# Performance work log

Measured on AMD Instinct MI355X. Metric: run time of the kernel, lower is better.

## Reference

```python
import jax, jax.numpy as jnp
import numpy as np

D_K, D_V, H, N = 128, 256, 256, 50
B, L = 128, 1024

def setup_inputs() -> dict:
    key = jax.random.key(0)
    ks = jax.random.split(key, 10)
    s = lambda fan_in: 1.0 / np.sqrt(fan_in)
    return {
        'problems': jax.random.normal(ks[0], (B, L, D_K), dtype=jnp.float32),
        'interactions': jax.random.normal(ks[1], (B, L, D_V), dtype=jnp.float32),
        'w_key': jax.random.uniform(ks[2], (N, D_K), jnp.float32, -s(D_K), s(D_K)),
        'w_erase_w': jax.random.uniform(ks[3], (D_V, D_V), jnp.float32, -s(D_V), s(D_V)),
        'w_erase_b': jax.random.uniform(ks[4], (D_V,), jnp.float32, -s(D_V), s(D_V)),
        'w_add_w': jax.random.uniform(ks[5], (D_V, D_V), jnp.float32, -s(D_V), s(D_V)),
        'w_add_b': jax.random.uniform(ks[6], (D_V,), jnp.float32, -s(D_V), s(D_V)),
        'w_out_w': jax.random.uniform(ks[7], (H, D_V + D_K), jnp.float32, -s(D_V + D_K), s(D_V + D_K)),
        'w_out_b': jax.random.uniform(ks[8], (H,), jnp.float32, -s(D_V + D_K), s(D_V + D_K)),
        'init_memory': jax.random.normal(ks[9], (N, D_V), dtype=jnp.float32),
    }

def reference(problems, interactions, w_key, w_erase_w, w_erase_b, w_add_w, w_add_b, w_out_w, w_out_b, init_memory):
    # Precompute per-step gates outside the scan (they do not depend on memory)
    e = jax.nn.sigmoid(jnp.einsum('bld,ed->ble', interactions, w_erase_w) + w_erase_b)  # (B,L,d_v)
    a = jnp.tanh(jnp.einsum('bld,ed->ble', interactions, w_add_w) + w_add_b)            # (B,L,d_v)
    score = jax.nn.softmax(jnp.einsum('bld,nd->bln', problems, w_key), axis=-1)          # (B,L,n)

    mem0 = jnp.broadcast_to(init_memory, (problems.shape[0], N, D_V))

    def step(memory, xs):
        sc_t, e_t, a_t = xs  # (B,n), (B,d_v), (B,d_v)
        read = jnp.einsum('bn,bnd->bd', sc_t, memory)  # weighted read
        memory = memory * (1.0 - sc_t[:, :, None] * e_t[:, None, :])
        memory = memory + sc_t[:, :, None] * a_t[:, None, :]
        return memory, read

    xs = (score.transpose(1, 0, 2), e.transpose(1, 0, 2), a.transpose(1, 0, 2))  # time-major
    _, reads = jax.lax.scan(step, mem0, xs)  # reads: (L,B,d_v)

    x = jnp.concatenate([reads.transpose(1, 0, 2), problems], axis=-1)  # (B,L,d_v+d_k)
    # dropout in eval mode = identity
    return jnp.tanh(jnp.einsum('blc,hc->blh', x, w_out_w) + w_out_b)
```

## Files before the change

### kernel.cpp

```cpp
#include <hip/hip_runtime.h>

#define B_    128
#define L_    1024
#define DK_   128
#define DV_   256
#define NS_   50
#define H_    256
#define M_    (B_ * L_)

typedef __attribute__((ext_vector_type(8))) short   short8;
typedef __attribute__((ext_vector_type(4))) float   float4v;
typedef __attribute__((ext_vector_type(2))) float   float2v;
typedef __attribute__((ext_vector_type(4))) int     int4v;

__device__ __forceinline__ float b2f(unsigned short u) {
    unsigned int x = ((unsigned int)u) << 16;
    return __builtin_bit_cast(float, x);
}
__device__ __forceinline__ unsigned short f2b(float f) {
    unsigned int x = __builtin_bit_cast(unsigned int, f);
    x += 0x7fffu + ((x >> 16) & 1u);
    return (unsigned short)(x >> 16);
}
__device__ __forceinline__ int pack2(float lo, float hi) {
    return (int)f2b(lo) | ((int)f2b(hi) << 16);
}
__device__ __forceinline__ float sigmoid_f(float x) {
    return 1.f / (1.f + __expf(-x));
}
__device__ __forceinline__ float tanh_f(float x) {
    return 1.f - 2.f / (__expf(2.f * x) + 1.f);
}

__global__ __launch_bounds__(256) void gate_kernel(
    const float* __restrict__ X,
    const float* __restrict__ We, const float* __restrict__ be,
    const float* __restrict__ Wa, const float* __restrict__ ba,
    unsigned short* __restrict__ e_out, unsigned short* __restrict__ a_out)
{
    constexpr int K = DV_;
    const int mblk = blockIdx.x, nblk = blockIdx.y, gate = blockIdx.z;
    const float* W    = gate ? Wa : We;
    const float* bias = gate ? ba : be;
    unsigned short* out = gate ? a_out : e_out;

    __shared__ unsigned short As[128 * 40];
    __shared__ unsigned short Bs[128 * 40];

    const int tid  = threadIdx.x;
    const int lane = tid & 63, wid = tid >> 6;
    const int wm = wid >> 1, wn = wid & 1;
    const int l15 = lane & 15, quad = lane >> 4;

    float4v acc[4][4];
#pragma unroll
    for (int i = 0; i < 4; i++)
#pragma unroll
        for (int j = 0; j < 4; j++) {
            acc[i][j][0] = 0.f; acc[i][j][1] = 0.f;
            acc[i][j][2] = 0.f; acc[i][j][3] = 0.f;
        }

    const int srow = tid >> 1;
    const int scol = (tid & 1) * 16;
    const size_t Abase = ((size_t)mblk * 128 + srow) * K;
    const size_t Bbase = ((size_t)nblk * 128 + srow) * K;

    for (int k0 = 0; k0 < K; k0 += 32) {
        const float* xa = &X[Abase + k0 + scol];
        const float* xb = &W[Bbase + k0 + scol];
        float4v va0 = *(const float4v*)(xa);
        float4v va1 = *(const float4v*)(xa + 4);
        float4v va2 = *(const float4v*)(xa + 8);
        float4v va3 = *(const float4v*)(xa + 12);
        float4v vb0 = *(const float4v*)(xb);
        float4v vb1 = *(const float4v*)(xb + 4);
        float4v vb2 = *(const float4v*)(xb + 8);
        float4v vb3 = *(const float4v*)(xb + 12);
        int4v pa0, pa1, pb0, pb1;
        pa0[0] = pack2(va0[0], va0[1]); pa0[1] = pack2(va0[2], va0[3]);
        pa0[2] = pack2(va1[0], va1[1]); pa0[3] = pack2(va1[2], va1[3]);
        pa1[0] = pack2(va2[0], va2[1]); pa1[1] = pack2(va2[2], va2[3]);
        pa1[2] = pack2(va3[0], va3[1]); pa1[3] = pack2(va3[2], va3[3]);
        pb0[0] = pack2(vb0[0], vb0[1]); pb0[1] = pack2(vb0[2], vb0[3]);
        pb0[2] = pack2(vb1[0], vb1[1]); pb0[3] = pack2(vb1[2], vb1[3]);
        pb1[0] = pack2(vb2[0], vb2[1]); pb1[1] = pack2(vb2[2], vb2[3]);
        pb1[2] = pack2(vb3[0], vb3[1]); pb1[3] = pack2(vb3[2], vb3[3]);
        *(int4v*)&As[srow * 40 + scol]     = pa0;
        *(int4v*)&As[srow * 40 + scol + 8] = pa1;
        *(int4v*)&Bs[srow * 40 + scol]     = pb0;
        *(int4v*)&Bs[srow * 40 + scol + 8] = pb1;
        __syncthreads();
        short8 af[4], bf[4];
#pragma unroll
        for (int i = 0; i < 4; i++)
            af[i] = *(const short8*)&As[(64 * wm + 16 * i + l15) * 40 + quad * 8];
#pragma unroll
        for (int j = 0; j < 4; j++)
            bf[j] = *(const short8*)&Bs[(64 * wn + 16 * j + l15) * 40 + quad * 8];
#pragma unroll
        for (int i = 0; i < 4; i++)
#pragma unroll
            for (int j = 0; j < 4; j++)
                acc[i][j] = __builtin_amdgcn_mfma_f32_16x16x32_bf16(af[i], bf[j], acc[i][j], 0, 0, 0);
        __syncthreads();
    }

#pragma unroll
    for (int i = 0; i < 4; i++) {
        const int row = mblk * 128 + 64 * wm + 16 * i + quad * 4;
#pragma unroll
        for (int j = 0; j < 4; j++) {
            const int col = nblk * 128 + 64 * wn + 16 * j + l15;
            const float bv = bias[col];
#pragma unroll
            for (int r = 0; r < 4; r++) {
                float v = acc[i][j][r] + bv;
                v = gate ? tanh_f(v) : sigmoid_f(v);
                out[(size_t)(row + r) * DV_ + col] = f2b(v);
            }
        }
    }
}

__global__ __launch_bounds__(256) void score_kernel(
    const float* __restrict__ problems,
    const float* __restrict__ w_key,
    float* __restrict__ score_scan)
{
    const int rowi = blockIdx.x * 256 + threadIdx.x;
    const float* p = problems + (size_t)rowi * DK_;

    float logit[NS_];
#pragma unroll
    for (int n = 0; n < NS_; n++) logit[n] = 0.f;

    for (int k0 = 0; k0 < DK_; k0 += 4) {
        float pf0 = p[k0], pf1 = p[k0+1], pf2 = p[k0+2], pf3 = p[k0+3];
#pragma unroll
        for (int n = 0; n < NS_; n++) {
            const float* wk = &w_key[n * DK_ + k0];
            logit[n] += pf0 * wk[0] + pf1 * wk[1] + pf2 * wk[2] + pf3 * wk[3];
        }
    }

    float mx = logit[0];
#pragma unroll
    for (int n = 1; n < NS_; n++) mx = fmaxf(mx, logit[n]);
    float sum = 0.f;
#pragma unroll
    for (int n = 0; n < NS_; n++) { logit[n] = __expf(logit[n] - mx); sum += logit[n]; }
    const float inv = 1.f / sum;

    float* o = score_scan + (size_t)rowi * 64;
#pragma unroll
    for (int v = 0; v < 16; v++) {
        float4v st;
#pragma unroll
        for (int c = 0; c < 4; c++) {
            const int j = v * 4 + c;
            st[c] = (j < NS_) ? logit[j] * inv : 0.f;
        }
        *(float4v*)(o + v * 4) = st;
    }
}

#define RCH 16

__global__ __launch_bounds__(512, 4) void scan_kernel(
    const float* __restrict__ score_scan,
    const unsigned short* __restrict__ e_buf,
    const unsigned short* __restrict__ a_buf,
    const float* __restrict__ init_mem,
    unsigned short* __restrict__ reads)
{
    __shared__ float r_s[8][RCH][64];

    const int b    = blockIdx.y;
    const int dblk = blockIdx.x;
    const int tid  = threadIdx.x;
    const int w    = tid >> 6;
    const int lane = tid & 63;
    const int d    = dblk * 64 + lane;

    float M[8];
#pragma unroll
    for (int i = 0; i < 8; i++) {
        const int n = w * 8 + i;
        M[i] = (n < NS_) ? init_mem[n * DV_ + d] : 0.f;
    }

    const size_t rb = (size_t)b * L_;
    const float* sbase = score_scan + rb * 64 + w * 8;
    const unsigned short* ep = e_buf + rb * DV_ + d;
    const unsigned short* ap = a_buf + rb * DV_ + d;

    float s_p[4][8];
    unsigned short e_p[8], a_p[8];

#pragma unroll
    for (int k = 0; k < 4; k++) {
        const float* sp = sbase + (size_t)k * 64;
        float4v x0 = *(const float4v*)(sp);
        float4v x1 = *(const float4v*)(sp + 4);
        s_p[k][0] = x0[0]; s_p[k][1] = x0[1]; s_p[k][2] = x0[2]; s_p[k][3] = x0[3];
        s_p[k][4] = x1[0]; s_p[k][5] = x1[1]; s_p[k][6] = x1[2]; s_p[k][7] = x1[3];
    }
#pragma unroll
    for (int k = 0; k < 8; k++) {
        e_p[k] = ep[(size_t)k * DV_];
        a_p[k] = ap[(size_t)k * DV_];
    }

    for (int t0 = 0; t0 < L_; t0 += RCH) {
#pragma unroll
        for (int u = 0; u < RCH; u++) {
            const float e_cur = b2f(e_p[u & 7]);
            const float a_cur = b2f(a_p[u & 7]);
            float r = 0.f;
#pragma unroll
            for (int i = 0; i < 8; i++) {
                const float s = s_p[u & 3][i];
                r = fmaf(s, M[i], r);
                M[i] = fmaf(s, fmaf(-e_cur, M[i], a_cur), M[i]);
            }
            r_s[w][u][lane] = r;
            {
                const float* sp = sbase + (size_t)(t0 + u + 4) * 64;
                float4v x0 = *(const float4v*)(sp);
                float4v x1 = *(const float4v*)(sp + 4);
                s_p[u & 3][0] = x0[0]; s_p[u & 3][1] = x0[1];
                s_p[u & 3][2] = x0[2]; s_p[u & 3][3] = x0[3];
                s_p[u & 3][4] = x1[0]; s_p[u & 3][5] = x1[1];
                s_p[u & 3][6] = x1[2]; s_p[u & 3][7] = x1[3];
            }
            e_p[u & 7] = ep[(size_t)(t0 + u + 8) * DV_];
            a_p[u & 7] = ap[(size_t)(t0 + u + 8) * DV_];
        }

        __syncthreads();
        {
            const int tt = tid >> 5;
            const int d0 = (tid & 31) * 2;
            float2v sm = *(const float2v*)&r_s[0][tt][d0];
#pragma unroll
            for (int ww = 1; ww < 8; ww++) {
                float2v v = *(const float2v*)&r_s[ww][tt][d0];
                sm[0] += v[0]; sm[1] += v[1];
            }
            *(unsigned int*)&reads[(rb + t0 + tt) * (size_t)DV_ + dblk * 64 + d0] =
                (unsigned int)pack2(sm[0], sm[1]);
        }
        __syncthreads();
    }
}

__global__ __launch_bounds__(256) void out_kernel(
    const unsigned short* __restrict__ reads,
    const float* __restrict__ problems,
    const float* __restrict__ Wo,
    const float* __restrict__ bo,
    float* __restrict__ out)
{
    constexpr int K = DV_ + DK_;
    const int mblk = blockIdx.x, nblk = blockIdx.y;

    __shared__ unsigned short As[128 * 40];
    __shared__ unsigned short Bs[128 * 40];

    const int tid  = threadIdx.x;
    const int lane = tid & 63, wid = tid >> 6;
    const int wm = wid >> 1, wn = wid & 1;
    const int l15 = lane & 15, quad = lane >> 4;

    float4v acc[4][4];
#pragma unroll
    for (int i = 0; i < 4; i++)
#pragma unroll
        for (int j = 0; j < 4; j++) {
            acc[i][j][0] = 0.f; acc[i][j][1] = 0.f;
            acc[i][j][2] = 0.f; acc[i][j][3] = 0.f;
        }

    const int srow = tid >> 1;
    const int scol = (tid & 1) * 16;
    const size_t mrow = (size_t)mblk * 128 + srow;
    const size_t brow = (size_t)nblk * 128 + srow;

    for (int k0 = 0; k0 < K; k0 += 32) {
        const int kk = k0 + scol;
        int4v a0, a1;
        if (kk < DV_) {
            a0 = *(const int4v*)&reads[mrow * DV_ + kk];
            a1 = *(const int4v*)&reads[mrow * DV_ + kk + 8];
        } else {
            const float* pr = &problems[mrow * DK_ + (kk - DV_)];
            float4v v0 = *(const float4v*)(pr);
            float4v v1 = *(const float4v*)(pr + 4);
            float4v v2 = *(const float4v*)(pr + 8);
            float4v v3 = *(const float4v*)(pr + 12);
            a0[0] = pack2(v0[0], v0[1]); a0[1] = pack2(v0[2], v0[3]);
            a0[2] = pack2(v1[0], v1[1]); a0[3] = pack2(v1[2], v1[3]);
            a1[0] = pack2(v2[0], v2[1]); a1[1] = pack2(v2[2], v2[3]);
            a1[2] = pack2(v3[0], v3[1]); a1[3] = pack2(v3[2], v3[3]);
        }
        const float* wb = &Wo[brow * K + kk];
        float4v u0 = *(const float4v*)(wb);
        float4v u1 = *(const float4v*)(wb + 4);
        float4v u2 = *(const float4v*)(wb + 8);
        float4v u3 = *(const float4v*)(wb + 12);
        int4v b0, b1;
        b0[0] = pack2(u0[0], u0[1]); b0[1] = pack2(u0[2], u0[3]);
        b0[2] = pack2(u1[0], u1[1]); b0[3] = pack2(u1[2], u1[3]);
        b1[0] = pack2(u2[0], u2[1]); b1[1] = pack2(u2[2], u2[3]);
        b1[2] = pack2(u3[0], u3[1]); b1[3] = pack2(u3[2], u3[3]);
        *(int4v*)&As[srow * 40 + scol]     = a0;
        *(int4v*)&As[srow * 40 + scol + 8] = a1;
        *(int4v*)&Bs[srow * 40 + scol]     = b0;
        *(int4v*)&Bs[srow * 40 + scol + 8] = b1;
        __syncthreads();
        short8 af[4], bf[4];
#pragma unroll
        for (int i = 0; i < 4; i++)
            af[i] = *(const short8*)&As[(64 * wm + 16 * i + l15) * 40 + quad * 8];
#pragma unroll
        for (int j = 0; j < 4; j++)
            bf[j] = *(const short8*)&Bs[(64 * wn + 16 * j + l15) * 40 + quad * 8];
#pragma unroll
        for (int i = 0; i < 4; i++)
#pragma unroll
            for (int j = 0; j < 4; j++)
                acc[i][j] = __builtin_amdgcn_mfma_f32_16x16x32_bf16(af[i], bf[j], acc[i][j], 0, 0, 0);
        __syncthreads();
    }

#pragma unroll
    for (int i = 0; i < 4; i++) {
        const int row = mblk * 128 + 64 * wm + 16 * i + quad * 4;
#pragma unroll
        for (int j = 0; j < 4; j++) {
            const int col = nblk * 128 + 64 * wn + 16 * j + l15;
            const float bv = bo[col];
#pragma unroll
            for (int r = 0; r < 4; r++) {
                out[(size_t)(row + r) * H_ + col] = tanh_f(acc[i][j][r] + bv);
            }
        }
    }
}

extern "C" void kernel_launch(void* const* d_in, const int* in_sizes, int n_in,
                              void* d_out, int out_size, void* d_ws, size_t ws_size,
                              hipStream_t stream) {
    const float* problems  = (const float*)d_in[0];
    const float* interact  = (const float*)d_in[1];
    const float* w_key     = (const float*)d_in[2];
    const float* w_erase_w = (const float*)d_in[3];
    const float* w_erase_b = (const float*)d_in[4];
    const float* w_add_w   = (const float*)d_in[5];
    const float* w_add_b   = (const float*)d_in[6];
    const float* w_out_w   = (const float*)d_in[7];
    const float* w_out_b   = (const float*)d_in[8];
    const float* init_mem  = (const float*)d_in[9];

    char* ws = (char*)d_ws;
    const size_t SZ_BF = (size_t)M_ * DV_ * 2;
    const size_t SZ_SC = (size_t)M_ * 64 * 4;
    unsigned short* e_buf = (unsigned short*)(ws);
    unsigned short* a_buf = (unsigned short*)(ws + SZ_BF);
    float*     score_scan = (float*)(ws + 2 * SZ_BF);
    unsigned short* reads = (unsigned short*)(ws + 2 * SZ_BF + SZ_SC);

    gate_kernel<<<dim3(M_ / 128, DV_ / 128, 2), 256, 0, stream>>>(
        interact, w_erase_w, w_erase_b, w_add_w, w_add_b, e_buf, a_buf);

    score_kernel<<<M_ / 256, 256, 0, stream>>>(problems, w_key, score_scan);

    scan_kernel<<<dim3(4, B_), 512, 0, stream>>>(
        score_scan, e_buf, a_buf, init_mem, reads);

    out_kernel<<<dim3(M_ / 128, H_ / 128), 256, 0, stream>>>(
        reads, problems, w_out_w, w_out_b, (float*)d_out);
}
```

Measured before the change: 952.5 us.

## Fuse erase/add gate GEMMs and stage scan gates via async LDS loads

The gate kernel now computes both the erase and add projections in one block, sharing the converted activation tile. This halves the fp32 reads and bf16 conversions of the interactions matrix, at the cost of double the accumulator registers. The scan kernel now copies e/a gate chunks of 64 steps into double-buffered LDS with global_load_lds. This replaces per-step scattered 2-byte global loads held in registers. The score prefetch depth also drops from 4 steps to 2, which may expose more load latency on the serial recurrence.

```diff
diff --git a/kernel.cpp b/kernel.cpp
--- a/kernel.cpp
+++ b/kernel.cpp
@@ -32,6 +32,12 @@
     return 1.f - 2.f / (__expf(2.f * x) + 1.f);
 }
 
+__device__ __forceinline__ void gload_lds16(const void* g, void* l) {
+    __builtin_amdgcn_global_load_lds(
+        (const __attribute__((address_space(1))) void*)g,
+        (__attribute__((address_space(3))) void*)l, 16, 0, 0);
+}
+
 __global__ __launch_bounds__(256) void gate_kernel(
     const float* __restrict__ X,
     const float* __restrict__ We, const float* __restrict__ be,
@@ -39,26 +45,26 @@
     unsigned short* __restrict__ e_out, unsigned short* __restrict__ a_out)
 {
     constexpr int K = DV_;
-    const int mblk = blockIdx.x, nblk = blockIdx.y, gate = blockIdx.z;
-    const float* W    = gate ? Wa : We;
-    const float* bias = gate ? ba : be;
-    unsigned short* out = gate ? a_out : e_out;
+    const int mblk = blockIdx.x, nblk = blockIdx.y;
 
     __shared__ unsigned short As[128 * 40];
-    __shared__ unsigned short Bs[128 * 40];
+    __shared__ unsigned short Be[128 * 40];
+    __shared__ unsigned short Ba[128 * 40];
 
     const int tid  = threadIdx.x;
     const int lane = tid & 63, wid = tid >> 6;
     const int wm = wid >> 1, wn = wid & 1;
     const int l15 = lane & 15, quad = lane >> 4;
 
-    float4v acc[4][4];
+    float4v acce[4][4], acca[4][4];
 #pragma unroll
     for (int i = 0; i < 4; i++)
 #pragma unroll
         for (int j = 0; j < 4; j++) {
-            acc[i][j][0] = 0.f; acc[i][j][1] = 0.f;
-            acc[i][j][2] = 0.f; acc[i][j][3] = 0.f;
+            acce[i][j][0] = 0.f; acce[i][j][1] = 0.f;
+            acce[i][j][2] = 0.f; acce[i][j][3] = 0.f;
+            acca[i][j][0] = 0.f; acca[i][j][1] = 0.f;
+            acca[i][j][2] = 0.f; acca[i][j][3] = 0.f;
         }
 
     const int srow = tid >> 1;
@@ -67,42 +73,75 @@
     const size_t Bbase = ((size_t)nblk * 128 + srow) * K;
 
     for (int k0 = 0; k0 < K; k0 += 32) {
-        const float* xa = &X[Abase + k0 + scol];
-        const float* xb = &W[Bbase + k0 + scol];
-        float4v va0 = *(const float4v*)(xa);
-        float4v va1 = *(const float4v*)(xa + 4);
-        float4v va2 = *(const float4v*)(xa + 8);
-        float4v va3 = *(const float4v*)(xa + 12);
-        float4v vb0 = *(const float4v*)(xb);
-        float4v vb1 = *(const float4v*)(xb + 4);
-        float4v vb2 = *(const float4v*)(xb + 8);
-        float4v vb3 = *(const float4v*)(xb + 12);
-        int4v pa0, pa1, pb0, pb1;
-        pa0[0] = pack2(va0[0], va0[1]); pa0[1] = pack2(va0[2], va0[3]);
-        pa0[2] = pack2(va1[0], va1[1]); pa0[3] = pack2(va1[2], va1[3]);
-        pa1[0] = pack2(va2[0], va2[1]); pa1[1] = pack2(va2[2], va2[3]);
-        pa1[2] = pack2(va3[0], va3[1]); pa1[3] = pack2(va3[2], va3[3]);
-        pb0[0] = pack2(vb0[0], vb0[1]); pb0[1] = pack2(vb0[2], vb0[3]);
-        pb0[2] = pack2(vb1[0], vb1[1]); pb0[3] = pack2(vb1[2], vb1[3]);
-        pb1[0] = pack2(vb2[0], vb2[1]); pb1[1] = pack2(vb2[2], vb2[3]);
-        pb1[2] = pack2(vb3[0], vb3[1]); pb1[3] = pack2(vb3[2], vb3[3]);
-        *(int4v*)&As[srow * 40 + scol]     = pa0;
-        *(int4v*)&As[srow * 40 + scol + 8] = pa1;
-        *(int4v*)&Bs[srow * 40 + scol]     = pb0;
-        *(int4v*)&Bs[srow * 40 + scol + 8] = pb1;
+        {
+            const float* xa = &X[Abase + k0 + scol];
+            float4v v0 = *(const float4v*)(xa);
+            float4v v1 = *(const float4v*)(xa + 4);
+            float4v v2 = *(const float4v*)(xa + 8);
+            float4v v3 = *(const float4v*)(xa + 12);
+            int4v p0, p1;
+            p0[0] = pack2(v0[0], v0[1]); p0[1] = pack2(v0[2], v0[3]);
+            p0[2] = pack2(v1[0], v1[1]); p0[3] = pack2(v1[2], v1[3]);
+            p1[0] = pack2(v2[0], v2[1]); p1[1] = pack2(v2[2], v2[3]);
+            p1[2] = pack2(v3[0], v3[1]); p1[3] = pack2(v3[2], v3[3]);
+            *(int4v*)&As[srow * 40 + scol]     = p0;
+            *(int4v*)&As[srow * 40 + scol + 8] = p1;
+        }
+        {
+            const float* wb = &We[Bbase + k0 + scol];
+            float4v v0 = *(const float4v*)(wb);
+            float4v v1 = *(const float4v*)(wb + 4);
+            float4v v2 = *(const float4v*)(wb + 8);
+            float4v v3 = *(const float4v*)(wb + 12);
+            int4v p0, p1;
+            p0[0] = pack2(v0[0], v0[1]); p0[1] = pack2(v0[2], v0[3]);
+            p0[2] = pack2(v1[0], v1[1]); p0[3] = pack2(v1[2], v1[3]);
+            p1[0] = pack2(v2[0], v2[1]); p1[1] = pack2(v2[2], v2[3]);
+            p1[2] = pack2(v3[0], v3[1]); p1[3] = pack2(v3[2], v3[3]);
+            *(int4v*)&Be[srow * 40 + scol]     = p0;
+            *(int4v*)&Be[srow * 40 + scol + 8] = p1;
+        }
+        {
+            const float* wb = &Wa[Bbase + k0 + scol];
+            float4v v0 = *(const float4v*)(wb);
+            float4v v1 = *(const float4v*)(wb + 4);
+            float4v v2 = *(const float4v*)(wb + 8);
+            float4v v3 = *(const float4v*)(wb + 12);
+            int4v p0, p1;
+            p0[0] = pack2(v0[0], v0[1]); p0[1] = pack2(v0[2], v0[3]);
+            p0[2] = pack2(v1[0], v1[1]); p0[3] = pack2(v1[2], v1[3]);
+            p1[0] = pack2(v2[0], v2[1]); p1[1] = pack2(v2[2], v2[3]);
+            p1[2] = pack2(v3[0], v3[1]); p1[3] = pack2(v3[2], v3[3]);
+            *(int4v*)&Ba[srow * 40 + scol]     = p0;
+            *(int4v*)&Ba[srow * 40 + scol + 8] = p1;
+        }
         __syncthreads();
-        short8 af[4], bf[4];
+        short8 af[4];
 #pragma unroll
         for (int i = 0; i < 4; i++)
             af[i] = *(const short8*)&As[(64 * wm + 16 * i + l15) * 40 + quad * 8];
-#pragma unroll
-        for (int j = 0; j < 4; j++)
-            bf[j] = *(const short8*)&Bs[(64 * wn + 16 * j + l15) * 40 + quad * 8];
-#pragma unroll
-        for (int i = 0; i < 4; i++)
+        {
+            short8 bf[4];
 #pragma unroll
             for (int j = 0; j < 4; j++)
-                acc[i][j] = __builtin_amdgcn_mfma_f32_16x16x32_bf16(af[i], bf[j], acc[i][j], 0, 0, 0);
+                bf[j] = *(const short8*)&Be[(64 * wn + 16 * j + l15) * 40 + quad * 8];
+#pragma unroll
+            for (int i = 0; i < 4; i++)
+#pragma unroll
+                for (int j = 0; j < 4; j++)
+                    acce[i][j] = __builtin_amdgcn_mfma_f32_16x16x32_bf16(af[i], bf[j], acce[i][j], 0, 0, 0);
+        }
+        {
+            short8 bf[4];
+#pragma unroll
+            for (int j = 0; j < 4; j++)
+                bf[j] = *(const short8*)&Ba[(64 * wn + 16 * j + l15) * 40 + quad * 8];
+#pragma unroll
+            for (int i = 0; i < 4; i++)
+#pragma unroll
+                for (int j = 0; j < 4; j++)
+                    acca[i][j] = __builtin_amdgcn_mfma_f32_16x16x32_bf16(af[i], bf[j], acca[i][j], 0, 0, 0);
+        }
         __syncthreads();
     }
 
@@ -112,12 +151,12 @@
 #pragma unroll
         for (int j = 0; j < 4; j++) {
             const int col = nblk * 128 + 64 * wn + 16 * j + l15;
-            const float bv = bias[col];
+            const float bve = be[col];
+            const float bva = ba[col];
 #pragma unroll
             for (int r = 0; r < 4; r++) {
-                float v = acc[i][j][r] + bv;
-                v = gate ? tanh_f(v) : sigmoid_f(v);
-                out[(size_t)(row + r) * DV_ + col] = f2b(v);
+                e_out[(size_t)(row + r) * DV_ + col] = f2b(sigmoid_f(acce[i][j][r] + bve));
+                a_out[(size_t)(row + r) * DV_ + col] = f2b(tanh_f(acca[i][j][r] + bva));
             }
         }
     }
@@ -165,6 +204,8 @@
     }
 }
 
+#define TCH 64
+#define NCH (L_ / TCH)
 #define RCH 16
 
 __global__ __launch_bounds__(512, 4) void scan_kernel(
@@ -174,85 +215,106 @@
     const float* __restrict__ init_mem,
     unsigned short* __restrict__ reads)
 {
-    __shared__ float r_s[8][RCH][64];
+    __shared__ unsigned short e_s[2][TCH][64];
+    __shared__ unsigned short a_s[2][TCH][64];
+    __shared__ float          r_s[8][RCH][64];
 
     const int b    = blockIdx.y;
     const int dblk = blockIdx.x;
     const int tid  = threadIdx.x;
     const int w    = tid >> 6;
+    const int wu   = __builtin_amdgcn_readfirstlane(w);
     const int lane = tid & 63;
     const int d    = dblk * 64 + lane;
 
     float M[8];
 #pragma unroll
     for (int i = 0; i < 8; i++) {
-        const int n = w * 8 + i;
+        const int n = wu * 8 + i;
         M[i] = (n < NS_) ? init_mem[n * DV_ + d] : 0.f;
     }
 
     const size_t rb = (size_t)b * L_;
-    const float* sbase = score_scan + rb * 64 + w * 8;
-    const unsigned short* ep = e_buf + rb * DV_ + d;
-    const unsigned short* ap = a_buf + rb * DV_ + d;
-
-    float s_p[4][8];
-    unsigned short e_p[8], a_p[8];
-
-#pragma unroll
-    for (int k = 0; k < 4; k++) {
-        const float* sp = sbase + (size_t)k * 64;
-        float4v x0 = *(const float4v*)(sp);
-        float4v x1 = *(const float4v*)(sp + 4);
-        s_p[k][0] = x0[0]; s_p[k][1] = x0[1]; s_p[k][2] = x0[2]; s_p[k][3] = x0[3];
-        s_p[k][4] = x1[0]; s_p[k][5] = x1[1]; s_p[k][6] = x1[2]; s_p[k][7] = x1[3];
-    }
-#pragma unroll
-    for (int k = 0; k < 8; k++) {
-        e_p[k] = ep[(size_t)k * DV_];
-        a_p[k] = ap[(size_t)k * DV_];
-    }
-
-    for (int t0 = 0; t0 < L_; t0 += RCH) {
-#pragma unroll
-        for (int u = 0; u < RCH; u++) {
-            const float e_cur = b2f(e_p[u & 7]);
-            const float a_cur = b2f(a_p[u & 7]);
-            float r = 0.f;
-#pragma unroll
-            for (int i = 0; i < 8; i++) {
-                const float s = s_p[u & 3][i];
-                r = fmaf(s, M[i], r);
-                M[i] = fmaf(s, fmaf(-e_cur, M[i], a_cur), M[i]);
+    const float* sbase = score_scan + rb * 64 + wu * 8;
+
+    auto stage = [&](int c, int p) {
+        const int tt = c * TCH + wu * 8 + (lane >> 3);
+        const size_t goff = (rb + tt) * (size_t)DV_ + dblk * 64 + (lane & 7) * 8;
+        gload_lds16(e_buf + goff, &e_s[p][wu * 8][0]);
+        gload_lds16(a_buf + goff, &a_s[p][wu * 8][0]);
+    };
+
+    float sc[8], sn[8];
+#define LOADS(dst, t) { \
+        const float* sp_ = sbase + (size_t)(t) * 64; \
+        const float4v x0_ = *(const float4v*)(sp_); \
+        const float4v x1_ = *(const float4v*)(sp_ + 4); \
+        dst[0]=x0_[0]; dst[1]=x0_[1]; dst[2]=x0_[2]; dst[3]=x0_[3]; \
+        dst[4]=x1_[0]; dst[5]=x1_[1]; dst[6]=x1_[2]; dst[7]=x1_[3]; }
+
+    int pp = 0;
+    stage(0, 0);
+    LOADS(sc, 0);
+    LOADS(sn, 1);
+    asm volatile("s_waitcnt vmcnt(0)" ::: "memory");
+    __syncthreads();
+
+    for (int c = 0; c < NCH; ++c) {
+        if (c + 1 < NCH) stage(c + 1, pp ^ 1);
+
+        for (int sub = 0; sub < TCH / RCH; ++sub) {
+            const int tb = c * TCH + sub * RCH;
+            const int lb = sub * RCH;
+#pragma unroll
+            for (int u = 0; u < RCH; u += 2) {
+                {
+                    const float e_cur = b2f(e_s[pp][lb + u][lane]);
+                    const float a_cur = b2f(a_s[pp][lb + u][lane]);
+                    float r = 0.f;
+#pragma unroll
+                    for (int i = 0; i < 8; i++) {
+                        const float s = sc[i];
+                        r = fmaf(s, M[i], r);
+                        M[i] = fmaf(s, fmaf(-e_cur, M[i], a_cur), M[i]);
+                    }
+                    r_s[w][u][lane] = r;
+                    LOADS(sc, tb + u + 2);
+                }
+                {
+                    const float e_cur = b2f(e_s[pp][lb + u + 1][lane]);
+                    const float a_cur = b2f(a_s[pp][lb + u + 1][lane]);
+                    float r = 0.f;
+#pragma unroll
+                    for (int i = 0; i < 8; i++) {
+                        const float s = sn[i];
+                        r = fmaf(s, M[i], r);
+                        M[i] = fmaf(s, fmaf(-e_cur, M[i], a_cur), M[i]);
+                    }
+                    r_s[w][u + 1][lane] = r;
+                    LOADS(sn, tb + u + 3);
+                }
             }
-            r_s[w][u][lane] = r;
+            __syncthreads();
             {
-                const float* sp = sbase + (size_t)(t0 + u + 4) * 64;
-                float4v x0 = *(const float4v*)(sp);
-                float4v x1 = *(const float4v*)(sp + 4);
-                s_p[u & 3][0] = x0[0]; s_p[u & 3][1] = x0[1];
-                s_p[u & 3][2] = x0[2]; s_p[u & 3][3] = x0[3];
-                s_p[u & 3][4] = x1[0]; s_p[u & 3][5] = x1[1];
-                s_p[u & 3][6] = x1[2]; s_p[u & 3][7] = x1[3];
+                const int tt = tid >> 5;
+                const int d0 = (tid & 31) * 2;
+                float2v sm = *(const float2v*)&r_s[0][tt][d0];
+#pragma unroll
+                for (int ww = 1; ww < 8; ww++) {
+                    float2v v = *(const float2v*)&r_s[ww][tt][d0];
+                    sm[0] += v[0]; sm[1] += v[1];
+                }
+                *(unsigned int*)&reads[(rb + tb + tt) * (size_t)DV_ + dblk * 64 + d0] =
+                    (unsigned int)pack2(sm[0], sm[1]);
             }
-            e_p[u & 7] = ep[(size_t)(t0 + u + 8) * DV_];
-            a_p[u & 7] = ap[(size_t)(t0 + u + 8) * DV_];
-        }
-
+            __syncthreads();
+        }
+
+        asm volatile("s_waitcnt vmcnt(0)" ::: "memory");
         __syncthreads();
-        {
-            const int tt = tid >> 5;
-            const int d0 = (tid & 31) * 2;
-            float2v sm = *(const float2v*)&r_s[0][tt][d0];
-#pragma unroll
-            for (int ww = 1; ww < 8; ww++) {
-                float2v v = *(const float2v*)&r_s[ww][tt][d0];
-                sm[0] += v[0]; sm[1] += v[1];
-            }
-            *(unsigned int*)&reads[(rb + t0 + tt) * (size_t)DV_ + dblk * 64 + d0] =
-                (unsigned int)pack2(sm[0], sm[1]);
-        }
-        __syncthreads();
-    }
+        pp ^= 1;
+    }
+#undef LOADS
 }
 
 __global__ __launch_bounds__(256) void out_kernel(
@@ -371,7 +433,7 @@
     float*     score_scan = (float*)(ws + 2 * SZ_BF);
     unsigned short* reads = (unsigned short*)(ws + 2 * SZ_BF + SZ_SC);
 
-    gate_kernel<<<dim3(M_ / 128, DV_ / 128, 2), 256, 0, stream>>>(
+    gate_kernel<<<dim3(M_ / 128, DV_ / 128), 256, 0, stream>>>(
         interact, w_erase_w, w_erase_b, w_add_w, w_add_b, e_buf, a_buf);
 
     score_kernel<<<M_ / 256, 256, 0, stream>>>(problems, w_key, score_scan);
```

Measured after the change: 832.2 us. 1.14x faster.
